# Kernel tuning notes

Hardware: AMD Instinct MI355X
Metric: run time of the kernel (lower is better)

The kernel has to match this reference:

```python
import jax, jax.numpy as jnp
import numpy as np

N = 50000
E = 800000
IN_DIM, HID, HEADS, OUT_DIM = 128, 32, 4, 16
NEG_SLOPE = 0.2


def gat_layer(x, src, dst, W, a_src, a_dst, bias, heads, out_ch, concat):
    # x: [N, F_in]; W: [F_in, heads*out_ch]; a_src/a_dst: [heads, out_ch]
    n = x.shape[0]
    xp = (x @ W).reshape(n, heads, out_ch)                      # [N, H, C]
    alpha_s = (xp * a_src).sum(-1)                              # [N, H]
    alpha_d = (xp * a_dst).sum(-1)                              # [N, H]
    e = jax.nn.leaky_relu(alpha_s[src] + alpha_d[dst], NEG_SLOPE)  # [E, H]
    # scatter-softmax over incoming edges of each destination node
    m = jax.ops.segment_max(e, dst, num_segments=n)             # [N, H]
    ex = jnp.exp(e - m[dst])
    denom = jax.ops.segment_sum(ex, dst, num_segments=n)        # [N, H]
    alpha = ex / denom[dst]                                     # [E, H]
    msg = xp[src] * alpha[:, :, None]                           # [E, H, C]
    out = jax.ops.segment_sum(msg, dst, num_segments=n)         # [N, H, C]
    if concat:
        return out.reshape(n, heads * out_ch) + bias
    return out.mean(axis=1) + bias


def setup_inputs() -> dict:
    key = jax.random.key(0)
    ks = jax.random.split(key, 10)
    x = jax.random.normal(ks[0], (N, IN_DIM), dtype=jnp.float32)
    edge_index = jax.random.randint(ks[1], (2, E), 0, N, dtype=jnp.int64)
    g = lambda k, shape, fan: jax.random.normal(k, shape, dtype=jnp.float32) * (1.0 / np.sqrt(fan))
    return {
        "x": x,
        "edge_index": edge_index,
        "W1": g(ks[2], (IN_DIM, HEADS * HID), IN_DIM),
        "a_src1": g(ks[3], (HEADS, HID), HID),
        "a_dst1": g(ks[4], (HEADS, HID), HID),
        "b1": jnp.zeros((HEADS * HID,), dtype=jnp.float32),
        "W2": g(ks[5], (HEADS * HID, OUT_DIM), HEADS * HID),
        "a_src2": g(ks[6], (1, OUT_DIM), OUT_DIM),
        "a_dst2": g(ks[7], (1, OUT_DIM), OUT_DIM),
        "b2": jnp.zeros((OUT_DIM,), dtype=jnp.float32),
    }


def reference(x, edge_index, W1, a_src1, a_dst1, b1, W2, a_src2, a_dst2, b2):
    # add self loops (PyG GATConv default add_self_loops=True)
    loop = jnp.arange(N, dtype=edge_index.dtype)
    src = jnp.concatenate([edge_index[0], loop])
    dst = jnp.concatenate([edge_index[1], loop])
    h = gat_layer(x, src, dst, W1, a_src1, a_dst1, b1, HEADS, HID, concat=True)
    h = jax.nn.elu(h)
    out = gat_layer(h, src, dst, W2, a_src2, a_dst2, b2, 1, OUT_DIM, concat=True)
    return jax.nn.log_softmax(out, axis=1)
```

## Files before the change

kernel.cpp:

```cpp
#include <hip/hip_runtime.h>
#include <math.h>

#define CAP    64
#define CAPB   32
#define GPART  256
#define BSH    7
#define BNODES 128

typedef __attribute__((ext_vector_type(4))) float f32x4;
typedef __attribute__((ext_vector_type(2))) float f32x2;
typedef __attribute__((ext_vector_type(8))) short s16x8;

__device__ __forceinline__ unsigned short f2bf(float f) {
    unsigned u = __float_as_uint(f);
    unsigned r = u + 0x7FFFu + ((u >> 16) & 1u);
    return (unsigned short)(r >> 16);
}
__device__ __forceinline__ float bf2f(unsigned short b) {
    return __uint_as_float(((unsigned)b) << 16);
}
__device__ __forceinline__ unsigned char f2fp8(float f) {
    int w = __builtin_amdgcn_cvt_pk_fp8_f32(f, f, 0, false);
    return (unsigned char)(w & 0xFF);
}

__device__ __forceinline__ int ldidx(const void* ei, int pos, bool i64) {
    if (i64) return (int)((const long long*)ei)[pos];
    return ((const int*)ei)[pos];
}

__global__ __launch_bounds__(256) void part_prep_k(
        const void* ei, const float* __restrict__ W1, const float* __restrict__ aS,
        const float* __restrict__ aD, unsigned short* __restrict__ Bt,
        int* __restrict__ stage, int* __restrict__ cnts, int E, int nbuk) {
    int blk = blockIdx.x, t = threadIdx.x;
    if (blk >= GPART) {
        int i = (blk - GPART) * 256 + t;
        if (i >= 144 * 128) return;
        int c = i >> 7, k = i & 127;
        float v = 0.f;
        if (c < 128) {
            v = W1[k * 128 + c];
        } else if (c < 136) {
            int q = c - 128;
            const float* a = (q < 4) ? aS : aD;
            int h = q & 3;
            float s = 0.f;
            for (int j = 0; j < 32; ++j)
                s = fmaf(W1[k * 128 + h * 32 + j], a[h * 32 + j], s);
            v = s;
        }
        Bt[c * 128 + k] = f2bf(v);
        return;
    }
    __shared__ int qcnt[1024];
    __shared__ int nz;
    if (t == 0) nz = 0;
    for (int b = t; b < nbuk; b += 256) qcnt[b] = 0;
    __syncthreads();
    int chunk = (E + GPART - 1) / GPART;
    int lo = blk * chunk;
    int hi = lo + chunk; if (hi > E) hi = E;
    int sidx = lo + t;
    if (sidx < hi && ((const unsigned*)ei)[2 * sidx + 1] != 0) atomicOr(&nz, 1);
    __syncthreads();
    bool i64 = (nz == 0);
    for (int i = lo + t; i < hi; i += 256) {
        int s = ldidx(ei, i, i64);
        int d = ldidx(ei, E + i, i64);
        int b = d >> BSH, dl = d & (BNODES - 1);
        int slot = atomicAdd(&qcnt[b], 1);
        if (slot < CAPB)
            stage[((size_t)b * GPART + blk) * CAPB + slot] = (dl << 24) | s;
    }
    __syncthreads();
    for (int b = t; b < nbuk; b += 256)
        cnts[b * GPART + blk] = min(qcnt[b], CAPB);
}

__global__ __launch_bounds__(512, 2) void gemm1_mfma(
        const float* __restrict__ x, const unsigned short* __restrict__ Bt,
        unsigned char* __restrict__ xp8, float* __restrict__ as1,
        float* __restrict__ ad1, int n) {
    __shared__ short xsb[128][132];
    __shared__ short btb[144][132];
    int tid = threadIdx.x;
    int rowbase = blockIdx.x * 128;

    {
        int row = tid >> 2, seg = tid & 3;
        int grow = rowbase + row; if (grow >= n) grow = n - 1;
        const float* xr = x + (size_t)grow * 128 + seg * 32;
#pragma unroll
        for (int q = 0; q < 8; ++q) {
            float4 c = *(const float4*)(xr + q * 4);
            short4 o;
            o.x = (short)f2bf(c.x); o.y = (short)f2bf(c.y);
            o.z = (short)f2bf(c.z); o.w = (short)f2bf(c.w);
            *(short4*)(&xsb[row][seg * 32 + q * 4]) = o;
        }
    }
    for (int idx = tid; idx < 144 * 32; idx += 512) {
        int c = idx >> 5, kq = idx & 31;
        short4 v = *(const short4*)(Bt + c * 128 + kq * 4);
        *(short4*)(&btb[c][kq * 4]) = v;
    }
    __syncthreads();

    int lane = tid & 63;
    int wave = tid >> 6;
    int rb = wave * 16;
    int col = lane & 15;
    int ksub = (lane >> 4) * 4;
    int arow = rb + (lane & 15);

    f32x4 acc[9];
#pragma unroll
    for (int t = 0; t < 9; ++t) acc[t] = (f32x4){0.f, 0.f, 0.f, 0.f};

#pragma unroll
    for (int ks = 0; ks < 4; ++ks) {
        short4 a0 = *(const short4*)(&xsb[arow][ks * 32 + ksub]);
        short4 a1 = *(const short4*)(&xsb[arow][ks * 32 + 16 + ksub]);
        s16x8 a;
        a[0] = a0.x; a[1] = a0.y; a[2] = a0.z; a[3] = a0.w;
        a[4] = a1.x; a[5] = a1.y; a[6] = a1.z; a[7] = a1.w;
#pragma unroll
        for (int t = 0; t < 9; ++t) {
            short4 b0 = *(const short4*)(&btb[t * 16 + col][ks * 32 + ksub]);
            short4 b1 = *(const short4*)(&btb[t * 16 + col][ks * 32 + 16 + ksub]);
            s16x8 b;
            b[0] = b0.x; b[1] = b0.y; b[2] = b0.z; b[3] = b0.w;
            b[4] = b1.x; b[5] = b1.y; b[6] = b1.z; b[7] = b1.w;
            acc[t] = __builtin_amdgcn_mfma_f32_16x16x32_bf16(a, b, acc[t], 0, 0, 0);
        }
    }

    int crow = rowbase + rb + (lane >> 4) * 4;
#pragma unroll
    for (int t = 0; t < 8; ++t) {
#pragma unroll
        for (int r = 0; r < 4; ++r) {
            int row = crow + r;
            if (row < n) xp8[(size_t)row * 128 + t * 16 + col] = f2fp8(acc[t][r]);
        }
    }
    if (col < 8) {
#pragma unroll
        for (int r = 0; r < 4; ++r) {
            int row = crow + r;
            if (row < n) {
                if (col < 4) as1[row * 4 + col] = acc[8][r];
                else         ad1[row * 4 + (col - 4)] = acc[8][r];
            }
        }
    }
}

__global__ __launch_bounds__(256) void merge_k(
        const int* __restrict__ cnts, const int* __restrict__ stage,
        int* __restrict__ src_pad, int* __restrict__ lens, int n) {
    __shared__ int rows[BNODES][CAP];
    __shared__ int rcnt[BNODES];
    int b = blockIdx.x, t = threadIdx.x;
    if (t < BNODES) rcnt[t] = 0;
    __syncthreads();
    int v = cnts[b * GPART + t];
    const int* seg = stage + ((size_t)b * GPART + t) * CAPB;
    for (int q = 0; q < v; ++q) {
        int item = seg[q];
        int dl = item >> 24;
        int s  = item & 0xFFFFFF;
        int r = atomicAdd(&rcnt[dl], 1);
        if (r < CAP - 1) rows[dl][r] = s;
    }
    __syncthreads();
    int base = b << BSH;
    if (t < BNODES && base + t < n) {
        int r = min(rcnt[t], CAP - 1);
        rows[t][r] = base + t;
        lens[base + t] = r + 1;
    }
    __syncthreads();
    for (int idx = t; idx < BNODES * CAP; idx += 256) {
        int node = base + (idx >> 6);
        if (node < n) src_pad[(size_t)node * CAP + (idx & (CAP - 1))] = rows[idx >> 6][idx & (CAP - 1)];
    }
}

__global__ __launch_bounds__(256) void agg1_proj_k(
        const int* __restrict__ lens, const int* __restrict__ src_pad,
        const float* __restrict__ as1, const float* __restrict__ ad1,
        const unsigned char* __restrict__ xp8, const float* __restrict__ b1,
        const float* __restrict__ W2, const float* __restrict__ aw_s,
        const float* __restrict__ aw_d, unsigned short* __restrict__ xp2b,
        float* __restrict__ as2, float* __restrict__ ad2, int n) {
    __shared__ unsigned short hs[8][128];
    int nodeblk = threadIdx.x >> 5;
    int g = blockIdx.x * 8 + nodeblk;
    int lane = threadIdx.x & 31;
    bool active = (g < n);
    int gg = active ? g : (n - 1);

    int h = lane >> 3;
    int len = active ? lens[gg] : 0;
    const int* sp = src_pad + (size_t)gg * CAP;
    float adv = ad1[gg * 4 + h];
    float ax = 0.f, ay = 0.f, az = 0.f, aw = 0.f, den = 0.f;
    int j = 0;
    int myq = lane & 7;
    int srcsel = (lane & 24);
    for (; j + 8 <= len; j += 8) {
        int ss[8];
#pragma unroll
        for (int q = 0; q < 8; ++q) ss[q] = sp[j + q];
        int s_my = sp[j + myq];
        float e_my = as1[s_my * 4 + h] + adv;
        e_my = e_my > 0.f ? e_my : 0.2f * e_my;
        e_my = __expf(e_my);
        unsigned vv[8];
#pragma unroll
        for (int q = 0; q < 8; ++q)
            vv[q] = *(const unsigned*)(xp8 + (size_t)ss[q] * 128 + lane * 4);
#pragma unroll
        for (int q = 0; q < 8; ++q) {
            float e = __shfl(e_my, srcsel | q, 32);
            den += e;
            f32x2 lo = __builtin_amdgcn_cvt_pk_f32_fp8(vv[q], false);
            f32x2 hi = __builtin_amdgcn_cvt_pk_f32_fp8(vv[q], true);
            ax = fmaf(lo[0], e, ax);
            ay = fmaf(lo[1], e, ay);
            az = fmaf(hi[0], e, az);
            aw = fmaf(hi[1], e, aw);
        }
    }
    for (; j < len; ++j) {
        int s = sp[j];
        float e = as1[s * 4 + h] + adv;
        e = e > 0.f ? e : 0.2f * e;
        e = __expf(e);
        unsigned w = *(const unsigned*)(xp8 + (size_t)s * 128 + lane * 4);
        den += e;
        f32x2 lo = __builtin_amdgcn_cvt_pk_f32_fp8(w, false);
        f32x2 hi = __builtin_amdgcn_cvt_pk_f32_fp8(w, true);
        ax = fmaf(lo[0], e, ax);
        ay = fmaf(lo[1], e, ay);
        az = fmaf(hi[0], e, az);
        aw = fmaf(hi[1], e, aw);
    }
    if (active) {
        float inv = 1.f / den;
        int c0 = lane * 4;
        const float4 bb = *(const float4*)(b1 + c0);
        float o0 = fmaf(ax, inv, bb.x); o0 = o0 > 0.f ? o0 : expm1f(o0);
        float o1 = fmaf(ay, inv, bb.y); o1 = o1 > 0.f ? o1 : expm1f(o1);
        float o2 = fmaf(az, inv, bb.z); o2 = o2 > 0.f ? o2 : expm1f(o2);
        float o3 = fmaf(aw, inv, bb.w); o3 = o3 > 0.f ? o3 : expm1f(o3);
        ushort4 o;
        o.x = f2bf(o0); o.y = f2bf(o1); o.z = f2bf(o2); o.w = f2bf(o3);
        *(ushort4*)(&hs[nodeblk][c0]) = o;
    }
    __syncthreads();
    if (!active) return;
    int jj = lane & 15, half = lane >> 4;
    float acc = 0.f;
    const unsigned short* hrow = &hs[nodeblk][half * 64];
    const float* w2p = W2 + (size_t)half * 64 * 16 + jj;
#pragma unroll 8
    for (int c = 0; c < 64; ++c)
        acc = fmaf(bf2f(hrow[c]), w2p[c * 16], acc);
    acc += __shfl_xor(acc, 16, 32);
    if (half == 0) xp2b[(size_t)g * 16 + jj] = f2bf(acc);
    float ps = acc * aw_s[jj];
    float pd = acc * aw_d[jj];
#pragma unroll
    for (int off = 8; off >= 1; off >>= 1) {
        ps += __shfl_xor(ps, off, 16);
        pd += __shfl_xor(pd, off, 16);
    }
    if (lane == 0) { as2[g] = ps; ad2[g] = pd; }
}

__global__ void agg2_gather(const int* __restrict__ lens, const int* __restrict__ src_pad,
                            const float* __restrict__ as2, const float* __restrict__ ad2,
                            const unsigned short* __restrict__ xp2b,
                            const float* __restrict__ b2,
                            float* __restrict__ out, int n) {
    int g = blockIdx.x * 64 + (threadIdx.x >> 2);
    if (g >= n) return;
    int lane = threadIdx.x & 3;
    int len = lens[g];
    const int* sp = src_pad + (size_t)g * CAP;
    float adv = ad2[g];
    float ax = 0.f, ay = 0.f, az = 0.f, aw = 0.f, den = 0.f;
    int j = 0;
    for (; j + 4 <= len; j += 4) {
        int s0 = sp[j + 0], s1 = sp[j + 1], s2 = sp[j + 2], s3 = sp[j + 3];
        float q0 = as2[s0], q1 = as2[s1], q2 = as2[s2], q3 = as2[s3];
        ushort4 v0 = *(const ushort4*)(xp2b + (size_t)s0 * 16 + lane * 4);
        ushort4 v1 = *(const ushort4*)(xp2b + (size_t)s1 * 16 + lane * 4);
        ushort4 v2 = *(const ushort4*)(xp2b + (size_t)s2 * 16 + lane * 4);
        ushort4 v3 = *(const ushort4*)(xp2b + (size_t)s3 * 16 + lane * 4);
        float e0 = q0 + adv; e0 = e0 > 0.f ? e0 : 0.2f * e0; e0 = __expf(e0);
        float e1 = q1 + adv; e1 = e1 > 0.f ? e1 : 0.2f * e1; e1 = __expf(e1);
        float e2 = q2 + adv; e2 = e2 > 0.f ? e2 : 0.2f * e2; e2 = __expf(e2);
        float e3 = q3 + adv; e3 = e3 > 0.f ? e3 : 0.2f * e3; e3 = __expf(e3);
        den += (e0 + e1) + (e2 + e3);
        ax = fmaf(bf2f(v0.x), e0, ax); ay = fmaf(bf2f(v0.y), e0, ay);
        az = fmaf(bf2f(v0.z), e0, az); aw = fmaf(bf2f(v0.w), e0, aw);
        ax = fmaf(bf2f(v1.x), e1, ax); ay = fmaf(bf2f(v1.y), e1, ay);
        az = fmaf(bf2f(v1.z), e1, az); aw = fmaf(bf2f(v1.w), e1, aw);
        ax = fmaf(bf2f(v2.x), e2, ax); ay = fmaf(bf2f(v2.y), e2, ay);
        az = fmaf(bf2f(v2.z), e2, az); aw = fmaf(bf2f(v2.w), e2, aw);
        ax = fmaf(bf2f(v3.x), e3, ax); ay = fmaf(bf2f(v3.y), e3, ay);
        az = fmaf(bf2f(v3.z), e3, az); aw = fmaf(bf2f(v3.w), e3, aw);
    }
    for (; j < len; ++j) {
        int s = sp[j];
        float e = as2[s] + adv;
        e = e > 0.f ? e : 0.2f * e;
        e = __expf(e);
        ushort4 v = *(const ushort4*)(xp2b + (size_t)s * 16 + lane * 4);
        den += e;
        ax = fmaf(bf2f(v.x), e, ax); ay = fmaf(bf2f(v.y), e, ay);
        az = fmaf(bf2f(v.z), e, az); aw = fmaf(bf2f(v.w), e, aw);
    }
    float inv = 1.f / den;
    const float4 bb = *(const float4*)(b2 + lane * 4);
    float v0 = fmaf(ax, inv, bb.x);
    float v1 = fmaf(ay, inv, bb.y);
    float v2 = fmaf(az, inv, bb.z);
    float v3 = fmaf(aw, inv, bb.w);
    float mm = fmaxf(fmaxf(v0, v1), fmaxf(v2, v3));
    for (int off = 1; off < 4; off <<= 1) mm = fmaxf(mm, __shfl_xor(mm, off, 4));
    float ss = __expf(v0 - mm) + __expf(v1 - mm) + __expf(v2 - mm) + __expf(v3 - mm);
    for (int off = 1; off < 4; off <<= 1) ss += __shfl_xor(ss, off, 4);
    float ls = mm + __logf(ss);
    float4 o = {v0 - ls, v1 - ls, v2 - ls, v3 - ls};
    *(float4*)(out + (size_t)g * 16 + lane * 4) = o;
}

extern "C" void kernel_launch(void* const* d_in, const int* in_sizes, int n_in,
                              void* d_out, int out_size, void* d_ws, size_t ws_size,
                              hipStream_t stream) {
    const float* x    = (const float*)d_in[0];
    const void*  ei   = d_in[1];
    const float* W1   = (const float*)d_in[2];
    const float* aS1  = (const float*)d_in[3];
    const float* aD1  = (const float*)d_in[4];
    const float* b1   = (const float*)d_in[5];
    const float* W2   = (const float*)d_in[6];
    const float* aS2  = (const float*)d_in[7];
    const float* aD2  = (const float*)d_in[8];
    const float* b2   = (const float*)d_in[9];

    const int N    = in_sizes[0] / 128;
    const int E    = in_sizes[1] / 2;
    const int NBUK = (N + BNODES - 1) >> BSH;

    char* p = (char*)d_ws;
    unsigned char* xp8 = (unsigned char*)p;     p += (size_t)128 * N;
    float* as1 = (float*)p;                     p += (size_t)4 * N * 4;
    float* ad1 = (float*)p;                     p += (size_t)4 * N * 4;
    unsigned short* xp2b = (unsigned short*)p;  p += (size_t)16 * N * 2;
    float* as2 = (float*)p;                     p += (size_t)N * 4;
    float* ad2 = (float*)p;                     p += (size_t)N * 4;
    int* lens = (int*)p;                        p += (size_t)N * 4;
    int* src_pad = (int*)p;                     p += (size_t)N * CAP * 4;
    int* stage = (int*)p;                       p += (size_t)NBUK * GPART * CAPB * 4;
    int* cnts = (int*)p;                        p += (size_t)NBUK * GPART * 4;
    unsigned short* Bt = (unsigned short*)p;    p += (size_t)144 * 128 * 2;

    const int PREPB = (144 * 128 + 255) / 256;

    part_prep_k<<<GPART + PREPB, 256, 0, stream>>>(ei, W1, aS1, aD1, Bt,
                                                   stage, cnts, E, NBUK);

    gemm1_mfma<<<(N + 127) / 128, 512, 0, stream>>>(x, Bt, xp8, as1, ad1, N);

    merge_k<<<NBUK, 256, 0, stream>>>(cnts, stage, src_pad, lens, N);

    agg1_proj_k<<<(N + 7) / 8, 256, 0, stream>>>(lens, src_pad, as1, ad1, xp8, b1,
                                                 W2, aS2, aD2, xp2b, as2, ad2, N);

    agg2_gather<<<(N + 63) / 64, 256, 0, stream>>>(lens, src_pad, as2, ad2, xp2b, b2,
                                                   (float*)d_out, N);
}
```

Baseline: 95.46 us.

## Assign one full wave per node in layer-1 aggregation, splitting edges across half-waves

The layer-1 aggregation kernel now maps each destination node to a full 64-lane wave instead of a 32-lane half. The two half-waves each process four of every eight neighbours and their partial sums are combined with a cross-half shuffle. The W2 projection is split into four 32-channel quarters. This doubles the parallelism per node to cut the serial gather-loop latency, at the cost of twice as many blocks, idle lanes in the epilogue, and extra shuffle reductions.

After: 100.3 us. +5.1%, slower.

```diff
diff --git a/kernel.cpp b/kernel.cpp
--- a/kernel.cpp
+++ b/kernel.cpp
@@ -195,35 +195,39 @@
         const float* __restrict__ W2, const float* __restrict__ aw_s,
         const float* __restrict__ aw_d, unsigned short* __restrict__ xp2b,
         float* __restrict__ as2, float* __restrict__ ad2, int n) {
-    __shared__ unsigned short hs[8][128];
-    int nodeblk = threadIdx.x >> 5;
-    int g = blockIdx.x * 8 + nodeblk;
-    int lane = threadIdx.x & 31;
+    __shared__ unsigned short hs[4][128];
+    int tid = threadIdx.x;
+    int wave = tid >> 6;
+    int lane = tid & 63;
+    int g = blockIdx.x * 4 + wave;
     bool active = (g < n);
     int gg = active ? g : (n - 1);
 
-    int h = lane >> 3;
+    int pair = lane >> 5;
+    int cl = lane & 31;
+    int h = cl >> 3;
     int len = active ? lens[gg] : 0;
     const int* sp = src_pad + (size_t)gg * CAP;
     float adv = ad1[gg * 4 + h];
     float ax = 0.f, ay = 0.f, az = 0.f, aw = 0.f, den = 0.f;
+    int myq = cl & 3;
+    int srcsel = cl & 24;
     int j = 0;
-    int myq = lane & 7;
-    int srcsel = (lane & 24);
     for (; j + 8 <= len; j += 8) {
-        int ss[8];
-#pragma unroll
-        for (int q = 0; q < 8; ++q) ss[q] = sp[j + q];
-        int s_my = sp[j + myq];
+        int base = j + pair * 4;
+        int s_my = sp[base + myq];
         float e_my = as1[s_my * 4 + h] + adv;
         e_my = e_my > 0.f ? e_my : 0.2f * e_my;
         e_my = __expf(e_my);
-        unsigned vv[8];
-#pragma unroll
-        for (int q = 0; q < 8; ++q)
-            vv[q] = *(const unsigned*)(xp8 + (size_t)ss[q] * 128 + lane * 4);
-#pragma unroll
-        for (int q = 0; q < 8; ++q) {
+        int ss[4];
+#pragma unroll
+        for (int q = 0; q < 4; ++q) ss[q] = sp[base + q];
+        unsigned vv[4];
+#pragma unroll
+        for (int q = 0; q < 4; ++q)
+            vv[q] = *(const unsigned*)(xp8 + (size_t)ss[q] * 128 + cl * 4);
+#pragma unroll
+        for (int q = 0; q < 4; ++q) {
             float e = __shfl(e_my, srcsel | q, 32);
             den += e;
             f32x2 lo = __builtin_amdgcn_cvt_pk_f32_fp8(vv[q], false);
@@ -234,12 +238,12 @@
             aw = fmaf(hi[1], e, aw);
         }
     }
-    for (; j < len; ++j) {
-        int s = sp[j];
+    for (int t = j + pair; t < len; t += 2) {
+        int s = sp[t];
         float e = as1[s * 4 + h] + adv;
         e = e > 0.f ? e : 0.2f * e;
         e = __expf(e);
-        unsigned w = *(const unsigned*)(xp8 + (size_t)s * 128 + lane * 4);
+        unsigned w = *(const unsigned*)(xp8 + (size_t)s * 128 + cl * 4);
         den += e;
         f32x2 lo = __builtin_amdgcn_cvt_pk_f32_fp8(w, false);
         f32x2 hi = __builtin_amdgcn_cvt_pk_f32_fp8(w, true);
@@ -248,9 +252,14 @@
         az = fmaf(hi[0], e, az);
         aw = fmaf(hi[1], e, aw);
     }
-    if (active) {
+    den += __shfl_xor(den, 32, 64);
+    ax  += __shfl_xor(ax, 32, 64);
+    ay  += __shfl_xor(ay, 32, 64);
+    az  += __shfl_xor(az, 32, 64);
+    aw  += __shfl_xor(aw, 32, 64);
+    if (active && pair == 0) {
         float inv = 1.f / den;
-        int c0 = lane * 4;
+        int c0 = cl * 4;
         const float4 bb = *(const float4*)(b1 + c0);
         float o0 = fmaf(ax, inv, bb.x); o0 = o0 > 0.f ? o0 : expm1f(o0);
         float o1 = fmaf(ay, inv, bb.y); o1 = o1 > 0.f ? o1 : expm1f(o1);
@@ -258,19 +267,20 @@
         float o3 = fmaf(aw, inv, bb.w); o3 = o3 > 0.f ? o3 : expm1f(o3);
         ushort4 o;
         o.x = f2bf(o0); o.y = f2bf(o1); o.z = f2bf(o2); o.w = f2bf(o3);
-        *(ushort4*)(&hs[nodeblk][c0]) = o;
+        *(ushort4*)(&hs[wave][c0]) = o;
     }
     __syncthreads();
     if (!active) return;
-    int jj = lane & 15, half = lane >> 4;
+    int jj = lane & 15, quarter = lane >> 4;
+    const unsigned short* hrow = &hs[wave][quarter * 32];
+    const float* w2p = W2 + (size_t)quarter * 32 * 16 + jj;
     float acc = 0.f;
-    const unsigned short* hrow = &hs[nodeblk][half * 64];
-    const float* w2p = W2 + (size_t)half * 64 * 16 + jj;
 #pragma unroll 8
-    for (int c = 0; c < 64; ++c)
+    for (int c = 0; c < 32; ++c)
         acc = fmaf(bf2f(hrow[c]), w2p[c * 16], acc);
-    acc += __shfl_xor(acc, 16, 32);
-    if (half == 0) xp2b[(size_t)g * 16 + jj] = f2bf(acc);
+    acc += __shfl_xor(acc, 16, 64);
+    acc += __shfl_xor(acc, 32, 64);
+    if (lane < 16) xp2b[(size_t)g * 16 + jj] = f2bf(acc);
     float ps = acc * aw_s[jj];
     float pd = acc * aw_d[jj];
 #pragma unroll
@@ -380,7 +390,7 @@
 
     merge_k<<<NBUK, 256, 0, stream>>>(cnts, stage, src_pad, lens, N);
 
-    agg1_proj_k<<<(N + 7) / 8, 256, 0, stream>>>(lens, src_pad, as1, ad1, xp8, b1,
+    agg1_proj_k<<<(N + 3) / 4, 256, 0, stream>>>(lens, src_pad, as1, ad1, xp8, b1,
                                                  W2, aS2, aD2, xp2b, as2, ad2, N);
 
     agg2_gather<<<(N + 63) / 64, 256, 0, stream>>>(lens, src_pad, as2, ad2, xp2b, b2,
```
